# Optimization experiments

Measured on AMD Instinct MI355X. Metric: run time of the kernel, lower is better.

## Reference

```python
import jax, jax.numpy as jnp
import numpy as np

N_NODES = 170000
N_EDGES = 1200000
IN_C, HID_C, OUT_C = 128, 128, 40
BN_EPS = 1e-5


def setup_inputs() -> dict:
    key = jax.random.key(0)
    ks = jax.random.split(key, 12)
    def glorot(k, fan_in, fan_out):
        lim = (6.0 / (fan_in + fan_out)) ** 0.5
        return jax.random.uniform(k, (fan_in, fan_out), jnp.float32, -lim, lim)
    x = jax.random.normal(ks[0], (N_NODES, IN_C), jnp.float32)
    edge_index = jax.random.randint(ks[1], (2, N_EDGES), 0, N_NODES, jnp.int64)
    return {
        "x": x,
        "edge_index": edge_index,
        "W0": glorot(ks[2], IN_C, HID_C), "b0": jnp.zeros((HID_C,), jnp.float32),
        "g0": jnp.ones((HID_C,), jnp.float32), "be0": jnp.zeros((HID_C,), jnp.float32),
        "W1": glorot(ks[3], HID_C, HID_C), "b1": jnp.zeros((HID_C,), jnp.float32),
        "g1": jnp.ones((HID_C,), jnp.float32), "be1": jnp.zeros((HID_C,), jnp.float32),
        "W2": glorot(ks[4], HID_C, OUT_C), "b2": jnp.zeros((OUT_C,), jnp.float32),
    }


def _gcn_norm(edge_index, num_nodes):
    # add self-loops, symmetric normalization (PyG GCNConv default)
    loop = jnp.arange(num_nodes, dtype=edge_index.dtype)
    src = jnp.concatenate([edge_index[0], loop])
    dst = jnp.concatenate([edge_index[1], loop])
    deg = jax.ops.segment_sum(jnp.ones_like(dst, jnp.float32), dst, num_segments=num_nodes)
    dinv = jnp.where(deg > 0, jax.lax.rsqrt(deg), 0.0)
    norm = dinv[src] * dinv[dst]  # [E+N]
    return src, dst, norm


def _conv(h, W, b, src, dst, norm, num_nodes):
    h = h @ W                              # [N, out]
    msg = h[src] * norm[:, None]           # gather + scale, [E+N, out]
    out = jax.ops.segment_sum(msg, dst, num_segments=num_nodes)
    return out + b


def _bn_relu(h, g, be):
    mean = jnp.mean(h, axis=0)
    var = jnp.mean(jnp.square(h - mean), axis=0)  # biased, as torch BN training
    h = (h - mean) * jax.lax.rsqrt(var + BN_EPS) * g + be
    return jax.nn.relu(h)


def reference(x, edge_index, W0, b0, g0, be0, W1, b1, g1, be1, W2, b2):
    N = x.shape[0]
    src, dst, norm = _gcn_norm(edge_index, N)
    h = _bn_relu(_conv(x, W0, b0, src, dst, norm, N), g0, be0)
    h = _bn_relu(_conv(h, W1, b1, src, dst, norm, N), g1, be1)
    return _conv(h, W2, b2, src, dst, norm, N)
```

## Files before the change

### kernel.cpp

```cpp
#include <hip/hip_runtime.h>

#define BN_EPS 1e-5f
#define CAP 3072

using bf16x8 = __attribute__((ext_vector_type(8))) short;
using f32x4  = __attribute__((ext_vector_type(4))) float;

__device__ __forceinline__ unsigned int f2bf(float f) {
    unsigned int u = __float_as_uint(f);
    u += 0x7fffu + ((u >> 16) & 1u);
    return u >> 16;
}
__device__ __forceinline__ float bflo(unsigned int u) { return __uint_as_float(u << 16); }
__device__ __forceinline__ float bfhi(unsigned int u) { return __uint_as_float(u & 0xffff0000u); }

__global__ __launch_bounds__(256) void k_bscatter(const int* __restrict__ ei,
                                                  int* __restrict__ bcur,
                                                  unsigned int* __restrict__ ebuf,
                                                  int E, int NB) {
    __shared__ int h[768];
    __shared__ int wb[768];
    for (int i = threadIdx.x; i < 768; i += 256) h[i] = 0;
    __syncthreads();
    int base = blockIdx.x * 8192;
    int rk[32];
    #pragma unroll
    for (int it = 0; it < 32; ++it) {
        int e = base + it * 256 + threadIdx.x;
        rk[it] = (e < E) ? atomicAdd(&h[ei[E + e] >> 8], 1) : 0;
    }
    __syncthreads();
    for (int i = threadIdx.x; i < NB; i += 256) {
        int c = h[i];
        wb[i] = c ? atomicAdd(&bcur[i], c) : 0;
    }
    __syncthreads();
    #pragma unroll
    for (int it = 0; it < 32; ++it) {
        int e = base + it * 256 + threadIdx.x;
        if (e < E) {
            unsigned s = (unsigned)ei[e], d = (unsigned)ei[E + e];
            int bk = (int)(d >> 8);
            int pos = wb[bk] + rk[it];
            if (pos < (bk + 1) * CAP)
                ebuf[pos] = s | ((d & 255u) << 24);
        }
    }
}

__global__ __launch_bounds__(256) void k_bfinal(const unsigned int* __restrict__ ebuf,
                                                const int* __restrict__ bcur,
                                                int* __restrict__ csr,
                                                int* __restrict__ rs,
                                                int* __restrict__ re,
                                                float* __restrict__ dinv, int N) {
    __shared__ int cnt[256];
    __shared__ int scn[256];
    __shared__ int cur[256];
    const int t = threadIdx.x, b = blockIdx.x;
    const int beg = b * CAP;
    const int cntE = min(bcur[b] - beg, CAP);
    cnt[t] = 0;
    __syncthreads();
    for (int j = t; j < cntE; j += 256)
        atomicAdd(&cnt[ebuf[beg + j] >> 24], 1);
    __syncthreads();
    int v = cnt[t];
    scn[t] = v;
    __syncthreads();
    for (int off = 1; off < 256; off <<= 1) {
        int x = (t >= off) ? scn[t - off] : 0;
        __syncthreads();
        scn[t] += x;
        __syncthreads();
    }
    int excl = scn[t] - v;
    int node = b * 256 + t;
    if (node < N) {
        rs[node]   = beg + excl;
        re[node]   = beg + excl + v;
        dinv[node] = rsqrtf((float)(1 + v));
    }
    cur[t] = beg + excl;
    __syncthreads();
    for (int j = t; j < cntE; j += 256) {
        unsigned e = ebuf[beg + j];
        int pos = atomicAdd(&cur[e >> 24], 1);
        csr[pos] = (int)(e & 0x00FFFFFFu);
    }
}

__global__ __launch_bounds__(256) void k_prepW3(const float* __restrict__ W0,
                                                const float* __restrict__ W1,
                                                const float* __restrict__ W2,
                                                unsigned short* __restrict__ Wf,
                                                int* __restrict__ bcur,
                                                float* __restrict__ stats, int NB) {
    int t = blockIdx.x * 256 + threadIdx.x;
    if (t < NB) bcur[t] = t * CAP;
    if (t < 512) stats[t] = 0.f;
    int wid = t >> 11;
    int f = t & 2047;
    const float* W = (wid == 0) ? W0 : (wid == 1) ? W1 : W2;
    int C = (wid == 2) ? 40 : 128;
    int lane = f & 63, frag = f >> 6;
    int kt = frag & 3, ct = frag >> 2;
    int r = lane & 15, q = lane >> 4;
    int col = ct * 16 + r;
    int kbase = kt * 32 + q * 8;
    unsigned int v[8];
    #pragma unroll
    for (int j = 0; j < 8; ++j)
        v[j] = (col < C) ? f2bf(W[(size_t)(kbase + j) * C + col]) : 0u;
    uint4 o;
    o.x = v[0] | (v[1] << 16);
    o.y = v[2] | (v[3] << 16);
    o.z = v[4] | (v[5] << 16);
    o.w = v[6] | (v[7] << 16);
    ((uint4*)Wf)[t] = o;
}

template <int NOCT, int OST>
__global__ __launch_bounds__(256) void k_gemm_mfma(
        const void* __restrict__ X, int xf32, const unsigned short* __restrict__ Wf,
        unsigned short* __restrict__ H, int N,
        const float* __restrict__ stats, const float* __restrict__ g,
        const float* __restrict__ be) {
    __shared__ unsigned short aF[16 * 512];
    __shared__ unsigned short bF[NOCT * 4 * 512];
    __shared__ float2 bnss[128];
    const int tid = threadIdx.x;
    const int rowbase = blockIdx.x * 64;

    if (stats && tid < 128) {
        const float invN = 1.0f / (float)N;
        float mean = stats[tid] * invN;
        float var  = fmaf(-mean, mean, stats[128 + tid] * invN);
        float sc   = g[tid] * rsqrtf(var + BN_EPS);
        bnss[tid]  = make_float2(sc, fmaf(-mean, sc, be[tid]));
    }

    {
        const uint4* src = (const uint4*)Wf;
        uint4* dst = (uint4*)bF;
        #pragma unroll
        for (int i = 0; i < NOCT; ++i) dst[tid + 256 * i] = src[tid + 256 * i];
    }
    __syncthreads();

    #pragma unroll
    for (int it = 0; it < 4; ++it) {
        int f = tid + 256 * it;
        int lane = f & 63, frag = f >> 6;
        int kt = frag & 3, rt = frag >> 2;
        int r = lane & 15, q = lane >> 4;
        int row = rowbase + rt * 16 + r;
        int kc = kt * 32 + q * 8;
        float vv[8];
        if (row < N) {
            if (xf32) {
                const float4* xp = (const float4*)((const float*)X + (size_t)row * 128 + kc);
                float4 p0 = xp[0], p1 = xp[1];
                vv[0] = p0.x; vv[1] = p0.y; vv[2] = p0.z; vv[3] = p0.w;
                vv[4] = p1.x; vv[5] = p1.y; vv[6] = p1.z; vv[7] = p1.w;
            } else {
                uint4 p = *((const uint4*)((const unsigned short*)X + (size_t)row * 128 + kc));
                vv[0] = bflo(p.x); vv[1] = bfhi(p.x);
                vv[2] = bflo(p.y); vv[3] = bfhi(p.y);
                vv[4] = bflo(p.z); vv[5] = bfhi(p.z);
                vv[6] = bflo(p.w); vv[7] = bfhi(p.w);
            }
            if (stats) {
                #pragma unroll
                for (int j = 0; j < 8; ++j) {
                    float2 ss = bnss[kc + j];
                    vv[j] = fmaxf(fmaf(vv[j], ss.x, ss.y), 0.0f);
                }
            }
        } else {
            #pragma unroll
            for (int j = 0; j < 8; ++j) vv[j] = 0.0f;
        }
        uint4 o;
        o.x = f2bf(vv[0]) | (f2bf(vv[1]) << 16);
        o.y = f2bf(vv[2]) | (f2bf(vv[3]) << 16);
        o.z = f2bf(vv[4]) | (f2bf(vv[5]) << 16);
        o.w = f2bf(vv[6]) | (f2bf(vv[7]) << 16);
        ((uint4*)aF)[f] = o;
    }
    __syncthreads();

    const int wave = tid >> 6, lane = tid & 63;
    f32x4 acc[NOCT];
    #pragma unroll
    for (int ct = 0; ct < NOCT; ++ct) acc[ct] = (f32x4){0.f, 0.f, 0.f, 0.f};

    #pragma unroll
    for (int kt = 0; kt < 4; ++kt) {
        bf16x8 a = ((const bf16x8*)aF)[(wave * 4 + kt) * 64 + lane];
        #pragma unroll
        for (int ct = 0; ct < NOCT; ++ct) {
            bf16x8 b = ((const bf16x8*)bF)[(ct * 4 + kt) * 64 + lane];
            acc[ct] = __builtin_amdgcn_mfma_f32_16x16x32_bf16(a, b, acc[ct], 0, 0, 0);
        }
    }

    const int q = lane >> 4, r = lane & 15;
    #pragma unroll
    for (int ct = 0; ct < NOCT; ++ct) {
        #pragma unroll
        for (int i = 0; i < 4; ++i) {
            int row = rowbase + wave * 16 + q * 4 + i;
            if (row < N)
                H[(size_t)row * OST + ct * 16 + r] = (unsigned short)f2bf(acc[ct][i]);
        }
    }
}

__global__ __launch_bounds__(256) void k_agg128(
        const unsigned short* __restrict__ H, const int* __restrict__ rs,
        const int* __restrict__ re, const int* __restrict__ csr,
        const float* __restrict__ dinv, const float* __restrict__ b,
        unsigned short* __restrict__ outb, int N) {
    int lane = threadIdx.x & 15;
    int node = blockIdx.x * 16 + (threadIdx.x >> 4);
    if (node >= N) return;
    float dd  = dinv[node];
    int   beg = rs[node];
    int   end = re[node];
    uint4 hp  = ((const uint4*)(H + (size_t)node * 128))[lane];
    float4 bb0 = ((const float4*)b)[lane * 2];
    float4 bb1 = ((const float4*)b)[lane * 2 + 1];
    float sl = dd * dd;
    float a0 = fmaf(bflo(hp.x), sl, bb0.x), a1 = fmaf(bfhi(hp.x), sl, bb0.y);
    float a2 = fmaf(bflo(hp.y), sl, bb0.z), a3 = fmaf(bfhi(hp.y), sl, bb0.w);
    float a4 = fmaf(bflo(hp.z), sl, bb1.x), a5 = fmaf(bfhi(hp.z), sl, bb1.y);
    float a6 = fmaf(bflo(hp.w), sl, bb1.z), a7 = fmaf(bfhi(hp.w), sl, bb1.w);
    int j = beg;
    for (; j + 2 <= end; j += 2) {
        int s0 = csr[j], s1 = csr[j + 1];
        float n0 = dinv[s0] * dd, n1 = dinv[s1] * dd;
        uint4 v0 = ((const uint4*)(H + (size_t)s0 * 128))[lane];
        uint4 v1 = ((const uint4*)(H + (size_t)s1 * 128))[lane];
        a0 = fmaf(bflo(v0.x), n0, fmaf(bflo(v1.x), n1, a0));
        a1 = fmaf(bfhi(v0.x), n0, fmaf(bfhi(v1.x), n1, a1));
        a2 = fmaf(bflo(v0.y), n0, fmaf(bflo(v1.y), n1, a2));
        a3 = fmaf(bfhi(v0.y), n0, fmaf(bfhi(v1.y), n1, a3));
        a4 = fmaf(bflo(v0.z), n0, fmaf(bflo(v1.z), n1, a4));
        a5 = fmaf(bfhi(v0.z), n0, fmaf(bfhi(v1.z), n1, a5));
        a6 = fmaf(bflo(v0.w), n0, fmaf(bflo(v1.w), n1, a6));
        a7 = fmaf(bfhi(v0.w), n0, fmaf(bfhi(v1.w), n1, a7));
    }
    if (j < end) {
        int s0 = csr[j];
        float n0 = dinv[s0] * dd;
        uint4 v0 = ((const uint4*)(H + (size_t)s0 * 128))[lane];
        a0 = fmaf(bflo(v0.x), n0, a0); a1 = fmaf(bfhi(v0.x), n0, a1);
        a2 = fmaf(bflo(v0.y), n0, a2); a3 = fmaf(bfhi(v0.y), n0, a3);
        a4 = fmaf(bflo(v0.z), n0, a4); a5 = fmaf(bfhi(v0.z), n0, a5);
        a6 = fmaf(bflo(v0.w), n0, a6); a7 = fmaf(bfhi(v0.w), n0, a7);
    }
    uint4 o;
    o.x = f2bf(a0) | (f2bf(a1) << 16);
    o.y = f2bf(a2) | (f2bf(a3) << 16);
    o.z = f2bf(a4) | (f2bf(a5) << 16);
    o.w = f2bf(a6) | (f2bf(a7) << 16);
    ((uint4*)(outb + (size_t)node * 128))[lane] = o;
}

__global__ __launch_bounds__(256) void k_agg40(
        const unsigned short* __restrict__ H, const int* __restrict__ rs,
        const int* __restrict__ re, const int* __restrict__ csr,
        const float* __restrict__ dinv, const float* __restrict__ b,
        float* __restrict__ out, int N) {
    int lane = threadIdx.x & 15;
    int node = blockIdx.x * 16 + (threadIdx.x >> 4);
    if (node >= N || lane >= 10) return;
    float dd  = dinv[node];
    int   beg = rs[node];
    int   end = re[node];
    uint2 hp  = ((const uint2*)(H + (size_t)node * 48))[lane];
    float4 bb = ((const float4*)b)[lane];
    float  sl = dd * dd;
    float4 acc = make_float4(fmaf(bflo(hp.x), sl, bb.x), fmaf(bfhi(hp.x), sl, bb.y),
                             fmaf(bflo(hp.y), sl, bb.z), fmaf(bfhi(hp.y), sl, bb.w));
    int j = beg;
    for (; j + 2 <= end; j += 2) {
        int s0 = csr[j], s1 = csr[j + 1];
        float n0 = dinv[s0] * dd, n1 = dinv[s1] * dd;
        uint2 v0 = ((const uint2*)(H + (size_t)s0 * 48))[lane];
        uint2 v1 = ((const uint2*)(H + (size_t)s1 * 48))[lane];
        acc.x = fmaf(bflo(v0.x), n0, fmaf(bflo(v1.x), n1, acc.x));
        acc.y = fmaf(bfhi(v0.x), n0, fmaf(bfhi(v1.x), n1, acc.y));
        acc.z = fmaf(bflo(v0.y), n0, fmaf(bflo(v1.y), n1, acc.z));
        acc.w = fmaf(bfhi(v0.y), n0, fmaf(bfhi(v1.y), n1, acc.w));
    }
    if (j < end) {
        int s0 = csr[j];
        float n0 = dinv[s0] * dd;
        uint2 v0 = ((const uint2*)(H + (size_t)s0 * 48))[lane];
        acc.x = fmaf(bflo(v0.x), n0, acc.x);
        acc.y = fmaf(bfhi(v0.x), n0, acc.y);
        acc.z = fmaf(bflo(v0.y), n0, acc.z);
        acc.w = fmaf(bfhi(v0.y), n0, acc.w);
    }
    ((float4*)(out + (size_t)node * 40))[lane] = acc;
}

__global__ __launch_bounds__(256) void k_bnstats(
        const unsigned short* __restrict__ Bb, float* __restrict__ stats, int N) {
    __shared__ float red[2][16][128];
    const int t = threadIdx.x;
    const int lane16 = t & 15, grp = t >> 4;
    const int cbase = lane16 * 8;
    float s[8], q[8];
    #pragma unroll
    for (int k = 0; k < 8; ++k) { s[k] = 0.f; q[k] = 0.f; }

    const int step = gridDim.x * 16;
    for (int r = blockIdx.x * 16 + grp; r < N; r += 2 * step) {
        uint4 p0 = *((const uint4*)(Bb + (size_t)r * 128 + cbase));
        int r1 = r + step;
        if (r1 < N) {
            uint4 p1 = *((const uint4*)(Bb + (size_t)r1 * 128 + cbase));
            float v[8] = {bflo(p1.x), bfhi(p1.x), bflo(p1.y), bfhi(p1.y),
                          bflo(p1.z), bfhi(p1.z), bflo(p1.w), bfhi(p1.w)};
            #pragma unroll
            for (int k = 0; k < 8; ++k) { s[k] += v[k]; q[k] = fmaf(v[k], v[k], q[k]); }
        }
        float u[8] = {bflo(p0.x), bfhi(p0.x), bflo(p0.y), bfhi(p0.y),
                      bflo(p0.z), bfhi(p0.z), bflo(p0.w), bfhi(p0.w)};
        #pragma unroll
        for (int k = 0; k < 8; ++k) { s[k] += u[k]; q[k] = fmaf(u[k], u[k], q[k]); }
    }
    #pragma unroll
    for (int k = 0; k < 8; ++k) {
        red[0][grp][cbase + k] = s[k];
        red[1][grp][cbase + k] = q[k];
    }
    __syncthreads();
    if (t < 128) {
        float acc = 0.f;
        #pragma unroll
        for (int g = 0; g < 16; ++g) acc += red[0][g][t];
        unsafeAtomicAdd(&stats[t], acc);
    } else {
        int c = t - 128;
        float acc = 0.f;
        #pragma unroll
        for (int g = 0; g < 16; ++g) acc += red[1][g][c];
        unsafeAtomicAdd(&stats[128 + c], acc);
    }
}

extern "C" void kernel_launch(void* const* d_in, const int* in_sizes, int n_in,
                              void* d_out, int out_size, void* d_ws, size_t ws_size,
                              hipStream_t stream) {
    const float* x   = (const float*)d_in[0];
    const int*   ei  = (const int*)d_in[1];
    const float* W0  = (const float*)d_in[2];
    const float* b0  = (const float*)d_in[3];
    const float* g0  = (const float*)d_in[4];
    const float* be0 = (const float*)d_in[5];
    const float* W1  = (const float*)d_in[6];
    const float* b1  = (const float*)d_in[7];
    const float* g1  = (const float*)d_in[8];
    const float* be1 = (const float*)d_in[9];
    const float* W2  = (const float*)d_in[10];
    const float* b2  = (const float*)d_in[11];
    float* out = (float*)d_out;

    const int N  = in_sizes[0] / 128;
    const int E  = in_sizes[1] / 2;
    const int NB = (N + 255) >> 8;
    const int EB = (E + 8191) / 8192;

    float* ws   = (float*)d_ws;
    size_t Npad = ((size_t)N + 511) & ~(size_t)511;
    size_t BCAP = (size_t)NB * CAP;
    float* dinv = ws;
    int*   rs   = (int*)(ws + Npad);
    int*   re   = rs + Npad;
    int*   csr  = re + Npad;
    unsigned int* ebuf = (unsigned int*)(csr + BCAP);
    int*   bcur = (int*)(ebuf + BCAP);
    float* stats0 = (float*)(bcur + 1024);
    float* stats1 = stats0 + 256;
    unsigned short* Wf = (unsigned short*)(stats1 + 256);
    unsigned short* Hb = Wf + 3 * 16384;
    unsigned short* Bb = Hb + Npad * 128;

    k_prepW3  <<<24, 256, 0, stream>>>(W0, W1, W2, Wf, bcur, stats0, NB);
    k_bscatter<<<EB, 256, 0, stream>>>(ei, bcur, ebuf, E, NB);
    k_bfinal  <<<NB, 256, 0, stream>>>(ebuf, bcur, csr, rs, re, dinv, N);

    int gemm_grid = (N + 63) / 64;
    int agg_grid  = (N + 15) / 16;

    k_gemm_mfma<8, 128><<<gemm_grid, 256, 0, stream>>>(x, 1, Wf, Hb, N,
                                                       nullptr, nullptr, nullptr);
    k_agg128<<<agg_grid, 256, 0, stream>>>(Hb, rs, re, csr, dinv, b0, Bb, N);
    k_bnstats<<<512, 256, 0, stream>>>(Bb, stats0, N);

    k_gemm_mfma<8, 128><<<gemm_grid, 256, 0, stream>>>(Bb, 0, Wf + 16384, Hb, N,
                                                       stats0, g0, be0);
    k_agg128<<<agg_grid, 256, 0, stream>>>(Hb, rs, re, csr, dinv, b1, Bb, N);
    k_bnstats<<<512, 256, 0, stream>>>(Bb, stats1, N);

    k_gemm_mfma<3, 48><<<gemm_grid, 256, 0, stream>>>(Bb, 0, Wf + 2 * 16384, Hb, N,
                                                      stats1, g1, be1);
    k_agg40<<<agg_grid, 256, 0, stream>>>(Hb, rs, re, csr, dinv, b2, out, N);
}
```

Before: 459.7 us.

## Load GEMM A fragments directly into registers and use packed bf16 conversion

The GEMM kernel now has each lane load its own A fragment rows from global memory straight into registers. This drops the shared-memory staging buffer and one block barrier, and out-of-range rows are clamped instead of zeroed. Float-to-bf16 rounding now uses the hardware packed convert instruction in both the GEMM and the 128-wide aggregation. The 40-column output stride is padded from 48 to 64 so gathered rows are better aligned. The trade-off is more direct global loads per lane and rows of the final layer's intermediate buffer that are 33% wider.

```diff
diff --git a/kernel.cpp b/kernel.cpp
--- a/kernel.cpp
+++ b/kernel.cpp
@@ -10,6 +10,11 @@
     unsigned int u = __float_as_uint(f);
     u += 0x7fffu + ((u >> 16) & 1u);
     return u >> 16;
+}
+__device__ __forceinline__ unsigned int f2bf2(float lo, float hi) {
+    unsigned int r;
+    asm("v_cvt_pk_bf16_f32 %0, %1, %2" : "=v"(r) : "v"(lo), "v"(hi));
+    return r;
 }
 __device__ __forceinline__ float bflo(unsigned int u) { return __uint_as_float(u << 16); }
 __device__ __forceinline__ float bfhi(unsigned int u) { return __uint_as_float(u & 0xffff0000u); }
@@ -126,7 +131,6 @@
         unsigned short* __restrict__ H, int N,
         const float* __restrict__ stats, const float* __restrict__ g,
         const float* __restrict__ be) {
-    __shared__ unsigned short aF[16 * 512];
     __shared__ unsigned short bF[NOCT * 4 * 512];
     __shared__ float2 bnss[128];
     const int tid = threadIdx.x;
@@ -139,7 +143,6 @@
         float sc   = g[tid] * rsqrtf(var + BN_EPS);
         bnss[tid]  = make_float2(sc, fmaf(-mean, sc, be[tid]));
     }
-
     {
         const uint4* src = (const uint4*)Wf;
         uint4* dst = (uint4*)bF;
@@ -148,71 +151,66 @@
     }
     __syncthreads();
 
-    #pragma unroll
-    for (int it = 0; it < 4; ++it) {
-        int f = tid + 256 * it;
-        int lane = f & 63, frag = f >> 6;
-        int kt = frag & 3, rt = frag >> 2;
-        int r = lane & 15, q = lane >> 4;
-        int row = rowbase + rt * 16 + r;
-        int kc = kt * 32 + q * 8;
+    const int wave = tid >> 6, lane = tid & 63;
+    const int r = lane & 15, q = lane >> 4;
+    const int row  = rowbase + wave * 16 + r;
+    const int rowc = min(row, N - 1);
+
+    bf16x8 afr[4];
+    #pragma unroll
+    for (int kt = 0; kt < 4; ++kt) {
+        const int kc = kt * 32 + q * 8;
         float vv[8];
-        if (row < N) {
-            if (xf32) {
-                const float4* xp = (const float4*)((const float*)X + (size_t)row * 128 + kc);
-                float4 p0 = xp[0], p1 = xp[1];
-                vv[0] = p0.x; vv[1] = p0.y; vv[2] = p0.z; vv[3] = p0.w;
-                vv[4] = p1.x; vv[5] = p1.y; vv[6] = p1.z; vv[7] = p1.w;
-            } else {
-                uint4 p = *((const uint4*)((const unsigned short*)X + (size_t)row * 128 + kc));
-                vv[0] = bflo(p.x); vv[1] = bfhi(p.x);
-                vv[2] = bflo(p.y); vv[3] = bfhi(p.y);
-                vv[4] = bflo(p.z); vv[5] = bfhi(p.z);
-                vv[6] = bflo(p.w); vv[7] = bfhi(p.w);
+        if (xf32) {
+            const float4* xp = (const float4*)((const float*)X + (size_t)rowc * 128 + kc);
+            float4 p0 = xp[0], p1 = xp[1];
+            vv[0] = p0.x; vv[1] = p0.y; vv[2] = p0.z; vv[3] = p0.w;
+            vv[4] = p1.x; vv[5] = p1.y; vv[6] = p1.z; vv[7] = p1.w;
+        } else {
+            uint4 p = *((const uint4*)((const unsigned short*)X + (size_t)rowc * 128 + kc));
+            vv[0] = bflo(p.x); vv[1] = bfhi(p.x);
+            vv[2] = bflo(p.y); vv[3] = bfhi(p.y);
+            vv[4] = bflo(p.z); vv[5] = bfhi(p.z);
+            vv[6] = bflo(p.w); vv[7] = bfhi(p.w);
+        }
+        if (stats) {
+            #pragma unroll
+            for (int j = 0; j < 8; ++j) {
+                float2 ss = bnss[kc + j];
+                vv[j] = fmaxf(fmaf(vv[j], ss.x, ss.y), 0.0f);
             }
-            if (stats) {
-                #pragma unroll
-                for (int j = 0; j < 8; ++j) {
-                    float2 ss = bnss[kc + j];
-                    vv[j] = fmaxf(fmaf(vv[j], ss.x, ss.y), 0.0f);
-                }
-            }
-        } else {
-            #pragma unroll
-            for (int j = 0; j < 8; ++j) vv[j] = 0.0f;
-        }
-        uint4 o;
-        o.x = f2bf(vv[0]) | (f2bf(vv[1]) << 16);
-        o.y = f2bf(vv[2]) | (f2bf(vv[3]) << 16);
-        o.z = f2bf(vv[4]) | (f2bf(vv[5]) << 16);
-        o.w = f2bf(vv[6]) | (f2bf(vv[7]) << 16);
-        ((uint4*)aF)[f] = o;
-    }
-    __syncthreads();
-
-    const int wave = tid >> 6, lane = tid & 63;
+        }
+        union { unsigned int u[4]; bf16x8 v; } pk;
+        pk.u[0] = f2bf2(vv[0], vv[1]);
+        pk.u[1] = f2bf2(vv[2], vv[3]);
+        pk.u[2] = f2bf2(vv[4], vv[5]);
+        pk.u[3] = f2bf2(vv[6], vv[7]);
+        afr[kt] = pk.v;
+    }
+
     f32x4 acc[NOCT];
     #pragma unroll
     for (int ct = 0; ct < NOCT; ++ct) acc[ct] = (f32x4){0.f, 0.f, 0.f, 0.f};
 
     #pragma unroll
     for (int kt = 0; kt < 4; ++kt) {
-        bf16x8 a = ((const bf16x8*)aF)[(wave * 4 + kt) * 64 + lane];
         #pragma unroll
         for (int ct = 0; ct < NOCT; ++ct) {
             bf16x8 b = ((const bf16x8*)bF)[(ct * 4 + kt) * 64 + lane];
-            acc[ct] = __builtin_amdgcn_mfma_f32_16x16x32_bf16(a, b, acc[ct], 0, 0, 0);
-        }
-    }
-
-    const int q = lane >> 4, r = lane & 15;
+            acc[ct] = __builtin_amdgcn_mfma_f32_16x16x32_bf16(afr[kt], b, acc[ct], 0, 0, 0);
+        }
+    }
+
     #pragma unroll
     for (int ct = 0; ct < NOCT; ++ct) {
         #pragma unroll
-        for (int i = 0; i < 4; ++i) {
-            int row = rowbase + wave * 16 + q * 4 + i;
-            if (row < N)
-                H[(size_t)row * OST + ct * 16 + r] = (unsigned short)f2bf(acc[ct][i]);
+        for (int i = 0; i < 4; i += 2) {
+            int row0 = rowbase + wave * 16 + q * 4 + i;
+            unsigned int pk = f2bf2(acc[ct][i], acc[ct][i + 1]);
+            if (row0 < N)
+                H[(size_t)row0 * OST + ct * 16 + r] = (unsigned short)pk;
+            if (row0 + 1 < N)
+                H[(size_t)(row0 + 1) * OST + ct * 16 + r] = (unsigned short)(pk >> 16);
         }
     }
 }
@@ -261,10 +259,10 @@
         a6 = fmaf(bflo(v0.w), n0, a6); a7 = fmaf(bfhi(v0.w), n0, a7);
     }
     uint4 o;
-    o.x = f2bf(a0) | (f2bf(a1) << 16);
-    o.y = f2bf(a2) | (f2bf(a3) << 16);
-    o.z = f2bf(a4) | (f2bf(a5) << 16);
-    o.w = f2bf(a6) | (f2bf(a7) << 16);
+    o.x = f2bf2(a0, a1);
+    o.y = f2bf2(a2, a3);
+    o.z = f2bf2(a4, a5);
+    o.w = f2bf2(a6, a7);
     ((uint4*)(outb + (size_t)node * 128))[lane] = o;
 }
 
@@ -279,7 +277,7 @@
     float dd  = dinv[node];
     int   beg = rs[node];
     int   end = re[node];
-    uint2 hp  = ((const uint2*)(H + (size_t)node * 48))[lane];
+    uint2 hp  = ((const uint2*)(H + (size_t)node * 64))[lane];
     float4 bb = ((const float4*)b)[lane];
     float  sl = dd * dd;
     float4 acc = make_float4(fmaf(bflo(hp.x), sl, bb.x), fmaf(bfhi(hp.x), sl, bb.y),
@@ -288,8 +286,8 @@
     for (; j + 2 <= end; j += 2) {
         int s0 = csr[j], s1 = csr[j + 1];
         float n0 = dinv[s0] * dd, n1 = dinv[s1] * dd;
-        uint2 v0 = ((const uint2*)(H + (size_t)s0 * 48))[lane];
-        uint2 v1 = ((const uint2*)(H + (size_t)s1 * 48))[lane];
+        uint2 v0 = ((const uint2*)(H + (size_t)s0 * 64))[lane];
+        uint2 v1 = ((const uint2*)(H + (size_t)s1 * 64))[lane];
         acc.x = fmaf(bflo(v0.x), n0, fmaf(bflo(v1.x), n1, acc.x));
         acc.y = fmaf(bfhi(v0.x), n0, fmaf(bfhi(v1.x), n1, acc.y));
         acc.z = fmaf(bflo(v0.y), n0, fmaf(bflo(v1.y), n1, acc.z));
@@ -298,7 +296,7 @@
     if (j < end) {
         int s0 = csr[j];
         float n0 = dinv[s0] * dd;
-        uint2 v0 = ((const uint2*)(H + (size_t)s0 * 48))[lane];
+        uint2 v0 = ((const uint2*)(H + (size_t)s0 * 64))[lane];
         acc.x = fmaf(bflo(v0.x), n0, acc.x);
         acc.y = fmaf(bfhi(v0.x), n0, acc.y);
         acc.z = fmaf(bflo(v0.y), n0, acc.z);
@@ -407,7 +405,7 @@
     k_agg128<<<agg_grid, 256, 0, stream>>>(Hb, rs, re, csr, dinv, b1, Bb, N);
     k_bnstats<<<512, 256, 0, stream>>>(Bb, stats1, N);
 
-    k_gemm_mfma<3, 48><<<gemm_grid, 256, 0, stream>>>(Bb, 0, Wf + 2 * 16384, Hb, N,
+    k_gemm_mfma<3, 64><<<gemm_grid, 256, 0, stream>>>(Bb, 0, Wf + 2 * 16384, Hb, N,
                                                       stats1, g1, be1);
     k_agg40<<<agg_grid, 256, 0, stream>>>(Hb, rs, re, csr, dinv, b2, out, N);
 }
```

Result: no change. 455.4 us (-0.9%).
